# Performance work log

Hardware: AMD Instinct MI355X
Metric: run time of the kernel (lower is better)

Reference implementation:

```python
import jax, jax.numpy as jnp
import numpy as np

NUM_HEAD = 8

def setup_inputs() -> dict:
    key = jax.random.key(0)
    ks = jax.random.split(key, 5)
    S, F, H = 4096, 1024, 1024
    scale = 0.02
    return {
        "x": jax.random.normal(ks[0], (1, S, F), dtype=jnp.float32),
        "Wq": jax.random.normal(ks[1], (F, H), dtype=jnp.float32) * scale,
        "Wk": jax.random.normal(ks[2], (F, H), dtype=jnp.float32) * scale,
        "Wv": jax.random.normal(ks[3], (F, H), dtype=jnp.float32) * scale,
        "Wo": jax.random.normal(ks[4], (H, F), dtype=jnp.float32) * scale,
    }

def reference(x, Wq, Wk, Wv, Wo):
    # x: [1, S, F]; weights applied as x @ W (torch Linear bias=False equivalent).
    # Dropout layers are treated as identity (eval mode) for determinism.
    B, S, F = x.shape
    H = Wq.shape[1]
    d_k = H // NUM_HEAD
    q = (x @ Wq).reshape(S, NUM_HEAD, d_k).transpose(1, 0, 2)  # [h, S, d_k]
    k = (x @ Wk).reshape(S, NUM_HEAD, d_k).transpose(1, 0, 2)
    v = (x @ Wv).reshape(S, NUM_HEAD, d_k).transpose(1, 0, 2)
    # Full attention matrix materialized, matching the original bmm-softmax-bmm.
    attn = jnp.einsum("hsd,htd->hst", q, k) / jnp.sqrt(jnp.float32(d_k))  # [h, S, S]
    attn = jax.nn.softmax(attn, axis=-1)
    y = jnp.einsum("hst,htd->hsd", attn, v)  # [h, S, d_k]
    y = y.transpose(1, 0, 2).reshape(1, S, H)  # [1, S, H]
    y = y @ Wo  # output projection [1, S, F]
    return (y, attn)
```

## Files before the change

kernel.cpp:

```cpp
#include <hip/hip_runtime.h>
#include <math.h>


typedef unsigned short u16;
typedef __attribute__((ext_vector_type(8))) short bf16x8;
typedef __attribute__((ext_vector_type(4))) float f32x4;

#define SEQ 4096
#define FDIM 1024
#define NHEAD 8
#define DK 128

__device__ __forceinline__ u16 f2bf(float f) {
  unsigned u = __float_as_uint(f);
  u += 0x7fffu + ((u >> 16) & 1u);
  return (u16)(u >> 16);
}
__device__ __forceinline__ float bf2f(u16 h) {
  return __uint_as_float(((unsigned)h) << 16);
}

__device__ __forceinline__ void g2l16(const void* g, void* l) {
  __builtin_amdgcn_global_load_lds(
      (const __attribute__((address_space(1))) void*)g,
      (__attribute__((address_space(3))) void*)l, 16, 0, 0);
}


__global__ void split_f32_bf16(const float4* __restrict__ in, u16* __restrict__ ohi,
                               u16* __restrict__ olo, int n4) {
  int i = blockIdx.x * 256 + threadIdx.x;
  if (i >= n4) return;
  float4 v = in[i];
  u16 h0 = f2bf(v.x), h1 = f2bf(v.y), h2 = f2bf(v.z), h3 = f2bf(v.w);
  u16 l0 = f2bf(v.x - bf2f(h0)), l1 = f2bf(v.y - bf2f(h1));
  u16 l2 = f2bf(v.z - bf2f(h2)), l3 = f2bf(v.w - bf2f(h3));
  *(ushort4*)(ohi + 4 * (size_t)i) = make_ushort4(h0, h1, h2, h3);
  *(ushort4*)(olo + 4 * (size_t)i) = make_ushort4(l0, l1, l2, l3);
}

__global__ void transpose_split_w(const float* __restrict__ in, u16* __restrict__ ohi,
                                  u16* __restrict__ olo, int dim, int do_split) {
  __shared__ float t[32][33];
  int tx = threadIdx.x, ty = threadIdx.y;
  int x = blockIdx.x * 32 + tx;
  int y0 = blockIdx.y * 32;
  for (int j = ty; j < 32; j += 8) t[j][tx] = in[(long)(y0 + j) * dim + x];
  __syncthreads();
  int x2 = y0 + tx;
  int y2 = blockIdx.x * 32;
  for (int j = ty; j < 32; j += 8) {
    float v = t[tx][j];
    u16 hi = f2bf(v);
    ohi[(long)(y2 + j) * dim + x2] = hi;
    if (do_split) olo[(long)(y2 + j) * dim + x2] = f2bf(v - bf2f(hi));
  }
}

__global__ void transpose_bf16(const u16* __restrict__ in, u16* __restrict__ out,
                               int rows, int cols) {
  __shared__ u16 t[32][33];
  int tx = threadIdx.x, ty = threadIdx.y;
  int x = blockIdx.x * 32 + tx;
  int y0 = blockIdx.y * 32;
  for (int j = ty; j < 32; j += 8) t[j][tx] = in[(long)(y0 + j) * cols + x];
  __syncthreads();
  int x2 = y0 + tx;
  int y2 = blockIdx.x * 32;
  for (int j = ty; j < 32; j += 8) out[(long)(y2 + j) * rows + x2] = t[tx][j];
}

__global__ void reciprocal_k(const float* __restrict__ in, float* __restrict__ out, int n) {
  int i = blockIdx.x * 256 + threadIdx.x;
  if (i < n) out[i] = 1.0f / in[i];
}

template <int BK, bool SPLIT, int EPI>
__global__ __launch_bounds__(256, 2) void gemm_bt(
    const u16* Ahi_, const u16* Alo_,
    const u16* Bhi_, const u16* Blo_,
    void* C0, void* C1,
    int Kdim, int lda, int ldb, int ldc,
    long aStrH, long bStrH, long cStrH) {
  constexpr int LDSN = 128 * BK;
  __shared__ u16 sAhi[LDSN];
  __shared__ u16 sBhi[LDSN];
  __shared__ u16 sAlo[SPLIT ? LDSN : 2];
  __shared__ u16 sBlo[SPLIT ? LDSN : 2];

  const int tid = threadIdx.x;
  const int lane = tid & 63;
  const int wave = tid >> 6;
  const int wr = wave >> 1, wc = wave & 1;
  const int quad = lane >> 4, l16 = lane & 15;
  const int h = blockIdx.z;
  const long bm = (long)blockIdx.y * 128;
  const long bn = (long)blockIdx.x * 128;

  const u16* Ahi = Ahi_ + (long)h * aStrH;
  const u16* Alo = SPLIT ? (Alo_ + (long)h * aStrH) : nullptr;
  const u16* Bhi = Bhi_ + (long)h * bStrH;
  const u16* Blo = SPLIT ? (Blo_ + (long)h * bStrH) : nullptr;

  f32x4 acc[4][4];
#pragma unroll
  for (int i = 0; i < 4; i++)
#pragma unroll
    for (int j = 0; j < 4; j++) acc[i][j] = (f32x4)0.0f;

  for (int k0 = 0; k0 < Kdim; k0 += BK) {
    constexpr int GR = (128 * BK) / (256 * 8);
#pragma unroll
    for (int r = 0; r < GR; ++r) {
      int e = (r * 256 + tid) * 8;
      int row = e / BK, col = e % BK;
      long ga = (bm + row) * (long)lda + k0 + col;
      long gb = (bn + row) * (long)ldb + k0 + col;
      g2l16(Ahi + ga, (char*)sAhi + (size_t)e * 2);
      g2l16(Bhi + gb, (char*)sBhi + (size_t)e * 2);
      if constexpr (SPLIT) {
        g2l16(Alo + ga, (char*)sAlo + (size_t)e * 2);
        g2l16(Blo + gb, (char*)sBlo + (size_t)e * 2);
      }
    }
    __syncthreads();

#pragma unroll
    for (int ks = 0; ks < BK; ks += 32) {
      bf16x8 aH[4], bH[4];
      bf16x8 aL[SPLIT ? 4 : 1], bL[SPLIT ? 4 : 1];
#pragma unroll
      for (int mi = 0; mi < 4; mi++) {
        int off = (wr * 64 + mi * 16 + l16) * BK + ks + quad * 8;
        aH[mi] = *(const bf16x8*)&sAhi[off];
        if constexpr (SPLIT) aL[mi] = *(const bf16x8*)&sAlo[off];
      }
#pragma unroll
      for (int ni = 0; ni < 4; ni++) {
        int off = (wc * 64 + ni * 16 + l16) * BK + ks + quad * 8;
        bH[ni] = *(const bf16x8*)&sBhi[off];
        if constexpr (SPLIT) bL[ni] = *(const bf16x8*)&sBlo[off];
      }
#pragma unroll
      for (int mi = 0; mi < 4; mi++)
#pragma unroll
        for (int ni = 0; ni < 4; ni++) {
          acc[mi][ni] = __builtin_amdgcn_mfma_f32_16x16x32_bf16(aH[mi], bH[ni], acc[mi][ni], 0, 0, 0);
          if constexpr (SPLIT) {
            acc[mi][ni] = __builtin_amdgcn_mfma_f32_16x16x32_bf16(aH[mi], bL[ni], acc[mi][ni], 0, 0, 0);
            acc[mi][ni] = __builtin_amdgcn_mfma_f32_16x16x32_bf16(aL[mi], bH[ni], acc[mi][ni], 0, 0, 0);
          }
        }
    }
    __syncthreads();
  }

  const long rowB = bm + wr * 64;
  const long colB = bn + wc * 64;
  if constexpr (EPI == 2) {
    u16* Chi = (u16*)C0 + (long)h * cStrH;
    u16* Clo = (u16*)C1 + (long)h * cStrH;
#pragma unroll
    for (int mi = 0; mi < 4; mi++)
#pragma unroll
      for (int ni = 0; ni < 4; ni++) {
        long col = colB + ni * 16 + l16;
#pragma unroll
        for (int r = 0; r < 4; r++) {
          long idx = (rowB + mi * 16 + quad * 4 + r) * (long)ldc + col;
          float v = acc[mi][ni][r];
          u16 hi = f2bf(v);
          Chi[idx] = hi;
          Clo[idx] = f2bf(v - bf2f(hi));
        }
      }
  } else if constexpr (EPI == 1) {
    u16* C = (u16*)C0 + (long)h * cStrH;
#pragma unroll
    for (int mi = 0; mi < 4; mi++)
#pragma unroll
      for (int ni = 0; ni < 4; ni++) {
        long col = colB + ni * 16 + l16;
#pragma unroll
        for (int r = 0; r < 4; r++)
          C[(rowB + mi * 16 + quad * 4 + r) * (long)ldc + col] = f2bf(acc[mi][ni][r]);
      }
  } else {
    float* C = (float*)C0 + (long)h * cStrH;
#pragma unroll
    for (int mi = 0; mi < 4; mi++)
#pragma unroll
      for (int ni = 0; ni < 4; ni++) {
        long col = colB + ni * 16 + l16;
#pragma unroll
        for (int r = 0; r < 4; r++)
          C[(rowB + mi * 16 + quad * 4 + r) * (long)ldc + col] = acc[mi][ni][r];
      }
  }
}

template <bool BF16S>
__global__ __launch_bounds__(256, 2) void qk_exp(
    const u16* __restrict__ Qhi, const u16* __restrict__ Qlo,
    const u16* __restrict__ Khi, const u16* __restrict__ Klo,
    void* __restrict__ outE, float* __restrict__ rowSum, float scale) {
  __shared__ u16 smem[32768];
  u16* sQh = smem;
  u16* sQl = smem + 8192;
  u16* sKh = smem + 16384;
  u16* sKl = smem + 24576;

  const int tid = threadIdx.x;
  const int lane = tid & 63, wave = tid >> 6;
  const int wr = wave >> 1, wc = wave & 1;
  const int quad = lane >> 4, l16 = lane & 15;
  const int h = blockIdx.z;
  const int bm = blockIdx.y * 128, bn = blockIdx.x * 128;
  const int colOff = h * DK;

  f32x4 acc[4][4];
#pragma unroll
  for (int i = 0; i < 4; i++)
#pragma unroll
    for (int j = 0; j < 4; j++) acc[i][j] = (f32x4)0.0f;

  for (int k0 = 0; k0 < DK; k0 += 64) {
#pragma unroll
    for (int r = 0; r < 4; ++r) {
      int e = (r * 256 + tid) * 8;
      int row = e >> 6, col = e & 63;
      long gq = (long)(bm + row) * FDIM + colOff + k0 + col;
      long gk = (long)(bn + row) * FDIM + colOff + k0 + col;
      g2l16(Qhi + gq, (char*)sQh + (size_t)e * 2);
      g2l16(Qlo + gq, (char*)sQl + (size_t)e * 2);
      g2l16(Khi + gk, (char*)sKh + (size_t)e * 2);
      g2l16(Klo + gk, (char*)sKl + (size_t)e * 2);
    }
    __syncthreads();
#pragma unroll
    for (int ks = 0; ks < 64; ks += 32) {
      bf16x8 aH[4], aL[4], bH[4], bL[4];
#pragma unroll
      for (int i = 0; i < 4; i++) {
        int offA = (wr * 64 + i * 16 + l16) * 64 + ks + quad * 8;
        int offB = (wc * 64 + i * 16 + l16) * 64 + ks + quad * 8;
        aH[i] = *(const bf16x8*)&sQh[offA];
        aL[i] = *(const bf16x8*)&sQl[offA];
        bH[i] = *(const bf16x8*)&sKh[offB];
        bL[i] = *(const bf16x8*)&sKl[offB];
      }
#pragma unroll
      for (int mi = 0; mi < 4; mi++)
#pragma unroll
        for (int ni = 0; ni < 4; ni++) {
          acc[mi][ni] = __builtin_amdgcn_mfma_f32_16x16x32_bf16(aH[mi], bH[ni], acc[mi][ni], 0, 0, 0);
          acc[mi][ni] = __builtin_amdgcn_mfma_f32_16x16x32_bf16(aH[mi], bL[ni], acc[mi][ni], 0, 0, 0);
          acc[mi][ni] = __builtin_amdgcn_mfma_f32_16x16x32_bf16(aL[mi], bH[ni], acc[mi][ni], 0, 0, 0);
        }
    }
    __syncthreads();
  }

#pragma unroll
  for (int mi = 0; mi < 4; mi++) {
    f32x4 rs = (f32x4)0.0f;
#pragma unroll
    for (int ni = 0; ni < 4; ni++)
#pragma unroll
      for (int r = 0; r < 4; r++) {
        float e = __expf(acc[mi][ni][r] * scale);
        acc[mi][ni][r] = e;
        rs[r] += e;
      }
#pragma unroll
    for (int m = 1; m < 16; m <<= 1) {
      rs[0] += __shfl_xor(rs[0], m);
      rs[1] += __shfl_xor(rs[1], m);
      rs[2] += __shfl_xor(rs[2], m);
      rs[3] += __shfl_xor(rs[3], m);
    }
    if (l16 == 0) {
      int rbase = h * SEQ + bm + wr * 64 + mi * 16 + quad * 4;
#pragma unroll
      for (int r = 0; r < 4; r++) atomicAdd(&rowSum[rbase + r], rs[r]);
    }
  }

  u16* P = smem;
#pragma unroll
  for (int mi = 0; mi < 4; mi++)
#pragma unroll
    for (int ni = 0; ni < 4; ni++)
#pragma unroll
      for (int r = 0; r < 4; r++)
        P[(wr * 64 + mi * 16 + quad * 4 + r) * 128 + wc * 64 + ni * 16 + l16] =
            f2bf(acc[mi][ni][r]);
  __syncthreads();

  if constexpr (BF16S) {
    u16* out = (u16*)outE + ((long)h << 24);
#pragma unroll
    for (int j = 0; j < 8; ++j) {
      int e = (j * 256 + tid) * 8;
      int row = e >> 7, col = e & 127;
      long g = (long)(bm + row) * SEQ + bn + col;
      *(uint4*)(out + g) = *(const uint4*)(P + e);
    }
  } else {
    float* out = (float*)outE + ((long)h << 24);
#pragma unroll
    for (int j = 0; j < 16; ++j) {
      int e = (j * 256 + tid) * 4;
      int row = e >> 7, col = e & 127;
      long g = (long)(bm + row) * SEQ + bn + col;
      ushort4 u = *(const ushort4*)(P + e);
      *(float4*)(out + g) = make_float4(bf2f(u.x), bf2f(u.y), bf2f(u.z), bf2f(u.w));
    }
  }
}

template <bool BF16S>
__global__ __launch_bounds__(256, 2) void pv_norm(
    const void* __restrict__ expS, const float* __restrict__ invRow,
    float* __restrict__ attnOut, const u16* __restrict__ Vt,
    u16* __restrict__ Yb) {
  __shared__ u16 sP[2][64 * 64];
  __shared__ u16 sV[2][128 * 64];
  const int tid = threadIdx.x;
  const int lane = tid & 63, wave = tid >> 6;
  const int wr = wave >> 1, wc = wave & 1;
  const int quad = lane >> 4, l16 = lane & 15;
  const int h = blockIdx.z;
  const int bm = blockIdx.y * 64;

  const int e0 = tid * 8, e1 = (256 + tid) * 8;
  const int row0 = e0 >> 6, col0 = e0 & 63;
  const int row1 = e1 >> 6, col1 = e1 & 63;
  const long arow0 = (long)h * SEQ + bm + row0;
  const long arow1 = (long)h * SEQ + bm + row1;
  const float inv0 = invRow[arow0];
  const float inv1 = invRow[arow1];

  f32x4 acc[2][4];
#pragma unroll
  for (int i = 0; i < 2; i++)
#pragma unroll
    for (int j = 0; j < 4; j++) acc[i][j] = (f32x4)0.0f;

  bf16x8 pbA0, pbA1, pbB0, pbB1;
  f32x4 pfA0, pfA1, pfA2, pfA3, pfB0, pfB1, pfB2, pfB3;

#define LOADP(S, k0)                                                           \
  do {                                                                         \
    if constexpr (BF16S) {                                                     \
      const u16* _s = (const u16*)expS;                                        \
      pb##S##0 = __builtin_nontemporal_load(                                   \
          (const bf16x8*)(_s + arow0 * SEQ + (k0) + col0));                    \
      pb##S##1 = __builtin_nontemporal_load(                                   \
          (const bf16x8*)(_s + arow1 * SEQ + (k0) + col1));                    \
    } else {                                                                   \
      const float* _s = (const float*)expS;                                    \
      pf##S##0 = __builtin_nontemporal_load(                                   \
          (const f32x4*)(_s + arow0 * SEQ + (k0) + col0));                     \
      pf##S##1 = __builtin_nontemporal_load(                                   \
          (const f32x4*)(_s + arow0 * SEQ + (k0) + col0 + 4));                 \
      pf##S##2 = __builtin_nontemporal_load(                                   \
          (const f32x4*)(_s + arow1 * SEQ + (k0) + col1));                     \
      pf##S##3 = __builtin_nontemporal_load(                                   \
          (const f32x4*)(_s + arow1 * SEQ + (k0) + col1 + 4));                 \
    }                                                                          \
  } while (0)

#define PROC(S, k0, buf)                                                       \
  do {                                                                         \
    float p0[8], p1[8];                                                        \
    if constexpr (BF16S) {                                                     \
      p0[0] = bf2f((u16)pb##S##0[0]) * inv0;                                   \
      p0[1] = bf2f((u16)pb##S##0[1]) * inv0;                                   \
      p0[2] = bf2f((u16)pb##S##0[2]) * inv0;                                   \
      p0[3] = bf2f((u16)pb##S##0[3]) * inv0;                                   \
      p0[4] = bf2f((u16)pb##S##0[4]) * inv0;                                   \
      p0[5] = bf2f((u16)pb##S##0[5]) * inv0;                                   \
      p0[6] = bf2f((u16)pb##S##0[6]) * inv0;                                   \
      p0[7] = bf2f((u16)pb##S##0[7]) * inv0;                                   \
      p1[0] = bf2f((u16)pb##S##1[0]) * inv1;                                   \
      p1[1] = bf2f((u16)pb##S##1[1]) * inv1;                                   \
      p1[2] = bf2f((u16)pb##S##1[2]) * inv1;                                   \
      p1[3] = bf2f((u16)pb##S##1[3]) * inv1;                                   \
      p1[4] = bf2f((u16)pb##S##1[4]) * inv1;                                   \
      p1[5] = bf2f((u16)pb##S##1[5]) * inv1;                                   \
      p1[6] = bf2f((u16)pb##S##1[6]) * inv1;                                   \
      p1[7] = bf2f((u16)pb##S##1[7]) * inv1;                                   \
    } else {                                                                   \
      p0[0] = pf##S##0[0] * inv0; p0[1] = pf##S##0[1] * inv0;                  \
      p0[2] = pf##S##0[2] * inv0; p0[3] = pf##S##0[3] * inv0;                  \
      p0[4] = pf##S##1[0] * inv0; p0[5] = pf##S##1[1] * inv0;                  \
      p0[6] = pf##S##1[2] * inv0; p0[7] = pf##S##1[3] * inv0;                  \
      p1[0] = pf##S##2[0] * inv1; p1[1] = pf##S##2[1] * inv1;                  \
      p1[2] = pf##S##2[2] * inv1; p1[3] = pf##S##2[3] * inv1;                  \
      p1[4] = pf##S##3[0] * inv1; p1[5] = pf##S##3[1] * inv1;                  \
      p1[6] = pf##S##3[2] * inv1; p1[7] = pf##S##3[3] * inv1;                  \
    }                                                                          \
    long _g0 = arow0 * SEQ + (k0) + col0;                                      \
    long _g1 = arow1 * SEQ + (k0) + col1;                                      \
    f32x4 _w0 = {p0[0], p0[1], p0[2], p0[3]};                                  \
    f32x4 _w1 = {p0[4], p0[5], p0[6], p0[7]};                                  \
    f32x4 _w2 = {p1[0], p1[1], p1[2], p1[3]};                                  \
    f32x4 _w3 = {p1[4], p1[5], p1[6], p1[7]};                                  \
    __builtin_nontemporal_store(_w0, (f32x4*)(attnOut + _g0));                 \
    __builtin_nontemporal_store(_w1, (f32x4*)(attnOut + _g0 + 4));             \
    __builtin_nontemporal_store(_w2, (f32x4*)(attnOut + _g1));                 \
    __builtin_nontemporal_store(_w3, (f32x4*)(attnOut + _g1 + 4));             \
    *(ushort4*)(sP[buf] + e0) =                                                \
        make_ushort4(f2bf(p0[0]), f2bf(p0[1]), f2bf(p0[2]), f2bf(p0[3]));      \
    *(ushort4*)(sP[buf] + e0 + 4) =                                            \
        make_ushort4(f2bf(p0[4]), f2bf(p0[5]), f2bf(p0[6]), f2bf(p0[7]));      \
    *(ushort4*)(sP[buf] + e1) =                                                \
        make_ushort4(f2bf(p1[0]), f2bf(p1[1]), f2bf(p1[2]), f2bf(p1[3]));      \
    *(ushort4*)(sP[buf] + e1 + 4) =                                            \
        make_ushort4(f2bf(p1[4]), f2bf(p1[5]), f2bf(p1[6]), f2bf(p1[7]));      \
  } while (0)

  auto STAGEV = [&](int k0, int buf) {
#pragma unroll
    for (int r = 0; r < 4; ++r) {
      int e = (r * 256 + tid) * 8;
      int row = e >> 6, col = e & 63;
      g2l16(Vt + (long)(h * DK + row) * SEQ + k0 + col,
            (char*)sV[buf] + (size_t)e * 2);
    }
  };

  auto DO_MFMA = [&](int buf) {
#pragma unroll
    for (int ks = 0; ks < 64; ks += 32) {
      bf16x8 a[2], b[4];
#pragma unroll
      for (int i = 0; i < 2; i++)
        a[i] = *(const bf16x8*)&sP[buf][(wr * 32 + i * 16 + l16) * 64 + ks + quad * 8];
#pragma unroll
      for (int i = 0; i < 4; i++)
        b[i] = *(const bf16x8*)&sV[buf][(wc * 64 + i * 16 + l16) * 64 + ks + quad * 8];
#pragma unroll
      for (int mi = 0; mi < 2; mi++)
#pragma unroll
        for (int ni = 0; ni < 4; ni++)
          acc[mi][ni] = __builtin_amdgcn_mfma_f32_16x16x32_bf16(a[mi], b[ni], acc[mi][ni], 0, 0, 0);
    }
  };

  LOADP(A, 0);
  STAGEV(0, 0);
  LOADP(B, 64);
  PROC(A, 0, 0);
  __syncthreads();

  for (int it = 0; it < 62; it += 2) {
    LOADP(A, (it + 2) * 64);
    STAGEV((it + 1) * 64, 1);
    DO_MFMA(0);
    PROC(B, (it + 1) * 64, 1);
    __syncthreads();
    LOADP(B, (it + 3) * 64);
    STAGEV((it + 2) * 64, 0);
    DO_MFMA(1);
    PROC(A, (it + 2) * 64, 0);
    __syncthreads();
  }
  STAGEV(63 * 64, 1);
  DO_MFMA(0);
  PROC(B, 63 * 64, 1);
  __syncthreads();
  DO_MFMA(1);

#undef LOADP
#undef PROC

#pragma unroll
  for (int mi = 0; mi < 2; mi++)
#pragma unroll
    for (int ni = 0; ni < 4; ni++)
#pragma unroll
      for (int r = 0; r < 4; r++) {
        long row = bm + wr * 32 + mi * 16 + quad * 4 + r;
        int col = h * DK + wc * 64 + ni * 16 + l16;
        Yb[row * (long)FDIM + col] = f2bf(acc[mi][ni][r]);
      }
}


extern "C" void kernel_launch(void* const* d_in, const int* in_sizes, int n_in,
                              void* d_out, int out_size, void* d_ws, size_t ws_size,
                              hipStream_t stream) {
  const float* x = (const float*)d_in[0];
  const float* Wq = (const float*)d_in[1];
  const float* Wk = (const float*)d_in[2];
  const float* Wv = (const float*)d_in[3];
  const float* Wo = (const float*)d_in[4];

  float* outY = (float*)d_out;
  float* attn = outY + (size_t)SEQ * FDIM;

  const size_t NX = (size_t)SEQ * FDIM;
  const size_t NW = (size_t)FDIM * FDIM;

  u16* p = (u16*)d_ws;
  u16* xhi = p; p += NX;
  u16* xlo = p; p += NX;
  u16* wqt_h = p; p += NW;
  u16* wqt_l = p; p += NW;
  u16* wkt_h = p; p += NW;
  u16* wkt_l = p; p += NW;
  u16* wvt = p; p += NW;
  u16* wot = p; p += NW;
  u16* Qhi = p; p += NX;
  u16* Qlo = p; p += NX;
  u16* Khi = p; p += NX;
  u16* Klo = p; p += NX;
  u16* Vb = p; p += NX;
  u16* Vt = p; p += NX;
  u16* Yb = p; p += NX;
  float* rowSum = (float*)p;
  float* invRow = rowSum + (size_t)NHEAD * SEQ;
  u16* expS = (u16*)(invRow + (size_t)NHEAD * SEQ);
  size_t need = (size_t)((char*)(expS + (size_t)NHEAD * SEQ * SEQ) - (char*)d_ws);
  bool bf16s = ws_size >= need;

  hipMemsetAsync(rowSum, 0, (size_t)NHEAD * SEQ * sizeof(float), stream);

  split_f32_bf16<<<dim3((NX / 4 + 255) / 256), 256, 0, stream>>>(
      (const float4*)x, xhi, xlo, NX / 4);

  dim3 tb(32, 8);
  transpose_split_w<<<dim3(32, 32), tb, 0, stream>>>(Wq, wqt_h, wqt_l, FDIM, 1);
  transpose_split_w<<<dim3(32, 32), tb, 0, stream>>>(Wk, wkt_h, wkt_l, FDIM, 1);
  transpose_split_w<<<dim3(32, 32), tb, 0, stream>>>(Wv, wvt, nullptr, FDIM, 0);
  transpose_split_w<<<dim3(32, 32), tb, 0, stream>>>(Wo, wot, nullptr, FDIM, 0);

  gemm_bt<32, true, 2><<<dim3(8, 32, 2), 256, 0, stream>>>(
      xhi, xlo, wqt_h, wqt_l, Qhi, Qlo,
      1024, 1024, 1024, 1024, 0, (long)2 * NW, (long)2 * NX);

  gemm_bt<64, false, 1><<<dim3(8, 32, 1), 256, 0, stream>>>(
      xhi, nullptr, wvt, nullptr, Vb, nullptr,
      1024, 1024, 1024, 1024, 0, 0, 0);
  transpose_bf16<<<dim3(32, 128), tb, 0, stream>>>(Vb, Vt, SEQ, FDIM);

  const float scale = 0.08838834764831845f;
  if (bf16s) {
    qk_exp<true><<<dim3(32, 32, NHEAD), 256, 0, stream>>>(
        Qhi, Qlo, Khi, Klo, expS, rowSum, scale);
  } else {
    qk_exp<false><<<dim3(32, 32, NHEAD), 256, 0, stream>>>(
        Qhi, Qlo, Khi, Klo, attn, rowSum, scale);
  }

  reciprocal_k<<<(NHEAD * SEQ + 255) / 256, 256, 0, stream>>>(rowSum, invRow, NHEAD * SEQ);

  if (bf16s) {
    pv_norm<true><<<dim3(1, 64, NHEAD), 256, 0, stream>>>(expS, invRow, attn, Vt, Yb);
  } else {
    pv_norm<false><<<dim3(1, 64, NHEAD), 256, 0, stream>>>(attn, invRow, attn, Vt, Yb);
  }

  gemm_bt<64, false, 0><<<dim3(8, 32, 1), 256, 0, stream>>>(
      Yb, nullptr, wot, nullptr, outY, nullptr,
      1024, 1024, 1024, 1024, 0, 0, 0);
}
```

Before: 1.170 ms.

## Split PV product into split-K GEMM, reduction, and separate attention normalization

On the bf16 path, the fused PV-and-normalize kernel is replaced by three kernels. First, a split-K GEMM over the unnormalized exp scores with larger 128-row tiles writes fp32 partials into the attn buffer as scratch. Second, a reduction applies the per-row reciprocal and converts to bf16. Third, a standalone streaming kernel writes the normalized fp32 attention matrix. This aims to raise parallelism and MFMA tile efficiency beyond the 512-block grid, at the cost of rereading expS, extra partial traffic, and more launches. The fp32 fallback pv_norm loses its double-buffered pipeline.

Measured after the change: 1.270 ms. +8.5%, slower.

```diff
diff --git a/kernel.cpp b/kernel.cpp
--- a/kernel.cpp
+++ b/kernel.cpp
@@ -4,12 +4,14 @@
 
 typedef unsigned short u16;
 typedef __attribute__((ext_vector_type(8))) short bf16x8;
+typedef __attribute__((ext_vector_type(8))) unsigned short u16x8;
 typedef __attribute__((ext_vector_type(4))) float f32x4;
 
 #define SEQ 4096
 #define FDIM 1024
 #define NHEAD 8
 #define DK 128
+#define KSPLIT 4
 
 __device__ __forceinline__ u16 f2bf(float f) {
   unsigned u = __float_as_uint(f);
@@ -319,13 +321,113 @@
   }
 }
 
+__global__ __launch_bounds__(256, 4) void pv_gemm(
+    const u16* __restrict__ expS, const u16* __restrict__ Vt,
+    float* __restrict__ ypart) {
+  __shared__ u16 sA[128 * 64];
+  __shared__ u16 sB[128 * 64];
+  const int tid = threadIdx.x;
+  const int lane = tid & 63, wave = tid >> 6;
+  const int wr = wave >> 1, wc = wave & 1;
+  const int quad = lane >> 4, l16 = lane & 15;
+  const int h = blockIdx.z;
+  const long bm = (long)blockIdx.y * 128;
+  const int kBase = blockIdx.x * (SEQ / KSPLIT);
+
+  const u16* A = expS + ((long)h << 24);
+  const u16* B = Vt + (long)h * DK * SEQ;
+
+  f32x4 acc[4][4];
+#pragma unroll
+  for (int i = 0; i < 4; i++)
+#pragma unroll
+    for (int j = 0; j < 4; j++) acc[i][j] = (f32x4)0.0f;
+
+  for (int k0 = kBase; k0 < kBase + SEQ / KSPLIT; k0 += 64) {
+#pragma unroll
+    for (int r = 0; r < 4; ++r) {
+      int e = (r * 256 + tid) * 8;
+      int row = e >> 6, col = e & 63;
+      g2l16(A + (bm + row) * (long)SEQ + k0 + col, (char*)sA + (size_t)e * 2);
+      g2l16(B + (long)row * SEQ + k0 + col, (char*)sB + (size_t)e * 2);
+    }
+    __syncthreads();
+#pragma unroll
+    for (int ks = 0; ks < 64; ks += 32) {
+      bf16x8 a[4], b[4];
+#pragma unroll
+      for (int mi = 0; mi < 4; mi++)
+        a[mi] = *(const bf16x8*)&sA[(wr * 64 + mi * 16 + l16) * 64 + ks + quad * 8];
+#pragma unroll
+      for (int ni = 0; ni < 4; ni++)
+        b[ni] = *(const bf16x8*)&sB[(wc * 64 + ni * 16 + l16) * 64 + ks + quad * 8];
+#pragma unroll
+      for (int mi = 0; mi < 4; mi++)
+#pragma unroll
+        for (int ni = 0; ni < 4; ni++)
+          acc[mi][ni] = __builtin_amdgcn_mfma_f32_16x16x32_bf16(a[mi], b[ni], acc[mi][ni], 0, 0, 0);
+    }
+    __syncthreads();
+  }
+
+  float* out = ypart + (long)blockIdx.x * ((long)SEQ * FDIM);
+#pragma unroll
+  for (int mi = 0; mi < 4; mi++)
+#pragma unroll
+    for (int ni = 0; ni < 4; ni++) {
+      int col = h * DK + wc * 64 + ni * 16 + l16;
+#pragma unroll
+      for (int r = 0; r < 4; r++) {
+        long row = bm + wr * 64 + mi * 16 + quad * 4 + r;
+        out[row * (long)FDIM + col] = acc[mi][ni][r];
+      }
+    }
+}
+
+__global__ void y_reduce_scale(const float* __restrict__ ypart,
+                               const float* __restrict__ invRow,
+                               u16* __restrict__ Yb) {
+  long i = ((long)blockIdx.x * 256 + threadIdx.x) * 4;
+  int s = (int)(i >> 10);
+  int f = (int)(i & 1023);
+  float inv = invRow[(f >> 7) * SEQ + s];
+  const long NP = (long)SEQ * FDIM;
+  f32x4 v = *(const f32x4*)(ypart + i);
+#pragma unroll
+  for (int ks = 1; ks < KSPLIT; ks++) v = v + *(const f32x4*)(ypart + ks * NP + i);
+  *(ushort4*)(Yb + i) =
+      make_ushort4(f2bf(v[0] * inv), f2bf(v[1] * inv), f2bf(v[2] * inv), f2bf(v[3] * inv));
+}
+
+__global__ void attn_norm(const u16* __restrict__ expS,
+                          const float* __restrict__ invRow,
+                          float* __restrict__ attn) {
+  const long TOT = ((long)NHEAD << 24) >> 4;
+  long c = (long)blockIdx.x * 256 + threadIdx.x;
+  const long stride = (long)gridDim.x * 256;
+  for (; c < TOT; c += stride) {
+    long flat = c << 4;
+    float inv = invRow[flat >> 12];
+    u16x8 v0 = __builtin_nontemporal_load((const u16x8*)(expS + flat));
+    u16x8 v1 = __builtin_nontemporal_load((const u16x8*)(expS + flat + 8));
+    f32x4 w0 = {bf2f(v0[0]) * inv, bf2f(v0[1]) * inv, bf2f(v0[2]) * inv, bf2f(v0[3]) * inv};
+    f32x4 w1 = {bf2f(v0[4]) * inv, bf2f(v0[5]) * inv, bf2f(v0[6]) * inv, bf2f(v0[7]) * inv};
+    f32x4 w2 = {bf2f(v1[0]) * inv, bf2f(v1[1]) * inv, bf2f(v1[2]) * inv, bf2f(v1[3]) * inv};
+    f32x4 w3 = {bf2f(v1[4]) * inv, bf2f(v1[5]) * inv, bf2f(v1[6]) * inv, bf2f(v1[7]) * inv};
+    __builtin_nontemporal_store(w0, (f32x4*)(attn + flat));
+    __builtin_nontemporal_store(w1, (f32x4*)(attn + flat + 4));
+    __builtin_nontemporal_store(w2, (f32x4*)(attn + flat + 8));
+    __builtin_nontemporal_store(w3, (f32x4*)(attn + flat + 12));
+  }
+}
+
 template <bool BF16S>
 __global__ __launch_bounds__(256, 2) void pv_norm(
     const void* __restrict__ expS, const float* __restrict__ invRow,
     float* __restrict__ attnOut, const u16* __restrict__ Vt,
     u16* __restrict__ Yb) {
-  __shared__ u16 sP[2][64 * 64];
-  __shared__ u16 sV[2][128 * 64];
+  __shared__ u16 sP[64 * 64];
+  __shared__ u16 sV[128 * 64];
   const int tid = threadIdx.x;
   const int lane = tid & 63, wave = tid >> 6;
   const int wr = wave >> 1, wc = wave & 1;
@@ -333,148 +435,63 @@
   const int h = blockIdx.z;
   const int bm = blockIdx.y * 64;
 
-  const int e0 = tid * 8, e1 = (256 + tid) * 8;
-  const int row0 = e0 >> 6, col0 = e0 & 63;
-  const int row1 = e1 >> 6, col1 = e1 & 63;
-  const long arow0 = (long)h * SEQ + bm + row0;
-  const long arow1 = (long)h * SEQ + bm + row1;
-  const float inv0 = invRow[arow0];
-  const float inv1 = invRow[arow1];
-
   f32x4 acc[2][4];
 #pragma unroll
   for (int i = 0; i < 2; i++)
 #pragma unroll
     for (int j = 0; j < 4; j++) acc[i][j] = (f32x4)0.0f;
 
-  bf16x8 pbA0, pbA1, pbB0, pbB1;
-  f32x4 pfA0, pfA1, pfA2, pfA3, pfB0, pfB1, pfB2, pfB3;
-
-#define LOADP(S, k0)                                                           \
-  do {                                                                         \
-    if constexpr (BF16S) {                                                     \
-      const u16* _s = (const u16*)expS;                                        \
-      pb##S##0 = __builtin_nontemporal_load(                                   \
-          (const bf16x8*)(_s + arow0 * SEQ + (k0) + col0));                    \
-      pb##S##1 = __builtin_nontemporal_load(                                   \
-          (const bf16x8*)(_s + arow1 * SEQ + (k0) + col1));                    \
-    } else {                                                                   \
-      const float* _s = (const float*)expS;                                    \
-      pf##S##0 = __builtin_nontemporal_load(                                   \
-          (const f32x4*)(_s + arow0 * SEQ + (k0) + col0));                     \
-      pf##S##1 = __builtin_nontemporal_load(                                   \
-          (const f32x4*)(_s + arow0 * SEQ + (k0) + col0 + 4));                 \
-      pf##S##2 = __builtin_nontemporal_load(                                   \
-          (const f32x4*)(_s + arow1 * SEQ + (k0) + col1));                     \
-      pf##S##3 = __builtin_nontemporal_load(                                   \
-          (const f32x4*)(_s + arow1 * SEQ + (k0) + col1 + 4));                 \
-    }                                                                          \
-  } while (0)
-
-#define PROC(S, k0, buf)                                                       \
-  do {                                                                         \
-    float p0[8], p1[8];                                                        \
-    if constexpr (BF16S) {                                                     \
-      p0[0] = bf2f((u16)pb##S##0[0]) * inv0;                                   \
-      p0[1] = bf2f((u16)pb##S##0[1]) * inv0;                                   \
-      p0[2] = bf2f((u16)pb##S##0[2]) * inv0;                                   \
-      p0[3] = bf2f((u16)pb##S##0[3]) * inv0;                                   \
-      p0[4] = bf2f((u16)pb##S##0[4]) * inv0;                                   \
-      p0[5] = bf2f((u16)pb##S##0[5]) * inv0;                                   \
-      p0[6] = bf2f((u16)pb##S##0[6]) * inv0;                                   \
-      p0[7] = bf2f((u16)pb##S##0[7]) * inv0;                                   \
-      p1[0] = bf2f((u16)pb##S##1[0]) * inv1;                                   \
-      p1[1] = bf2f((u16)pb##S##1[1]) * inv1;                                   \
-      p1[2] = bf2f((u16)pb##S##1[2]) * inv1;                                   \
-      p1[3] = bf2f((u16)pb##S##1[3]) * inv1;                                   \
-      p1[4] = bf2f((u16)pb##S##1[4]) * inv1;                                   \
-      p1[5] = bf2f((u16)pb##S##1[5]) * inv1;                                   \
-      p1[6] = bf2f((u16)pb##S##1[6]) * inv1;                                   \
-      p1[7] = bf2f((u16)pb##S##1[7]) * inv1;                                   \
-    } else {                                                                   \
-      p0[0] = pf##S##0[0] * inv0; p0[1] = pf##S##0[1] * inv0;                  \
-      p0[2] = pf##S##0[2] * inv0; p0[3] = pf##S##0[3] * inv0;                  \
-      p0[4] = pf##S##1[0] * inv0; p0[5] = pf##S##1[1] * inv0;                  \
-      p0[6] = pf##S##1[2] * inv0; p0[7] = pf##S##1[3] * inv0;                  \
-      p1[0] = pf##S##2[0] * inv1; p1[1] = pf##S##2[1] * inv1;                  \
-      p1[2] = pf##S##2[2] * inv1; p1[3] = pf##S##2[3] * inv1;                  \
-      p1[4] = pf##S##3[0] * inv1; p1[5] = pf##S##3[1] * inv1;                  \
-      p1[6] = pf##S##3[2] * inv1; p1[7] = pf##S##3[3] * inv1;                  \
-    }                                                                          \
-    long _g0 = arow0 * SEQ + (k0) + col0;                                      \
-    long _g1 = arow1 * SEQ + (k0) + col1;                                      \
-    f32x4 _w0 = {p0[0], p0[1], p0[2], p0[3]};                                  \
-    f32x4 _w1 = {p0[4], p0[5], p0[6], p0[7]};                                  \
-    f32x4 _w2 = {p1[0], p1[1], p1[2], p1[3]};                                  \
-    f32x4 _w3 = {p1[4], p1[5], p1[6], p1[7]};                                  \
-    __builtin_nontemporal_store(_w0, (f32x4*)(attnOut + _g0));                 \
-    __builtin_nontemporal_store(_w1, (f32x4*)(attnOut + _g0 + 4));             \
-    __builtin_nontemporal_store(_w2, (f32x4*)(attnOut + _g1));                 \
-    __builtin_nontemporal_store(_w3, (f32x4*)(attnOut + _g1 + 4));             \
-    *(ushort4*)(sP[buf] + e0) =                                                \
-        make_ushort4(f2bf(p0[0]), f2bf(p0[1]), f2bf(p0[2]), f2bf(p0[3]));      \
-    *(ushort4*)(sP[buf] + e0 + 4) =                                            \
-        make_ushort4(f2bf(p0[4]), f2bf(p0[5]), f2bf(p0[6]), f2bf(p0[7]));      \
-    *(ushort4*)(sP[buf] + e1) =                                                \
-        make_ushort4(f2bf(p1[0]), f2bf(p1[1]), f2bf(p1[2]), f2bf(p1[3]));      \
-    *(ushort4*)(sP[buf] + e1 + 4) =                                            \
-        make_ushort4(f2bf(p1[4]), f2bf(p1[5]), f2bf(p1[6]), f2bf(p1[7]));      \
-  } while (0)
-
-  auto STAGEV = [&](int k0, int buf) {
+  for (int k0 = 0; k0 < SEQ; k0 += 64) {
+#pragma unroll
+    for (int c = 0; c < 2; ++c) {
+      int e = (c * 256 + tid) * 8;
+      int row = e >> 6, col = e & 63;
+      long arow = (long)h * SEQ + bm + row;
+      long g = arow * SEQ + k0 + col;
+      float inv = invRow[arow];
+      float p[8];
+      if constexpr (BF16S) {
+        ushort4 u0 = *(const ushort4*)((const u16*)expS + g);
+        ushort4 u1 = *(const ushort4*)((const u16*)expS + g + 4);
+        p[0] = bf2f(u0.x) * inv; p[1] = bf2f(u0.y) * inv;
+        p[2] = bf2f(u0.z) * inv; p[3] = bf2f(u0.w) * inv;
+        p[4] = bf2f(u1.x) * inv; p[5] = bf2f(u1.y) * inv;
+        p[6] = bf2f(u1.z) * inv; p[7] = bf2f(u1.w) * inv;
+      } else {
+        float4 f0 = *(const float4*)((const float*)expS + g);
+        float4 f1 = *(const float4*)((const float*)expS + g + 4);
+        p[0] = f0.x * inv; p[1] = f0.y * inv; p[2] = f0.z * inv; p[3] = f0.w * inv;
+        p[4] = f1.x * inv; p[5] = f1.y * inv; p[6] = f1.z * inv; p[7] = f1.w * inv;
+      }
+      *(float4*)(attnOut + g) = make_float4(p[0], p[1], p[2], p[3]);
+      *(float4*)(attnOut + g + 4) = make_float4(p[4], p[5], p[6], p[7]);
+      *(ushort4*)(sP + e) = make_ushort4(f2bf(p[0]), f2bf(p[1]), f2bf(p[2]), f2bf(p[3]));
+      *(ushort4*)(sP + e + 4) = make_ushort4(f2bf(p[4]), f2bf(p[5]), f2bf(p[6]), f2bf(p[7]));
+    }
 #pragma unroll
     for (int r = 0; r < 4; ++r) {
       int e = (r * 256 + tid) * 8;
       int row = e >> 6, col = e & 63;
-      g2l16(Vt + (long)(h * DK + row) * SEQ + k0 + col,
-            (char*)sV[buf] + (size_t)e * 2);
-    }
-  };
-
-  auto DO_MFMA = [&](int buf) {
+      g2l16(Vt + (long)(h * DK + row) * SEQ + k0 + col, (char*)sV + (size_t)e * 2);
+    }
+    __syncthreads();
 #pragma unroll
     for (int ks = 0; ks < 64; ks += 32) {
       bf16x8 a[2], b[4];
 #pragma unroll
       for (int i = 0; i < 2; i++)
-        a[i] = *(const bf16x8*)&sP[buf][(wr * 32 + i * 16 + l16) * 64 + ks + quad * 8];
+        a[i] = *(const bf16x8*)&sP[(wr * 32 + i * 16 + l16) * 64 + ks + quad * 8];
 #pragma unroll
       for (int i = 0; i < 4; i++)
-        b[i] = *(const bf16x8*)&sV[buf][(wc * 64 + i * 16 + l16) * 64 + ks + quad * 8];
+        b[i] = *(const bf16x8*)&sV[(wc * 64 + i * 16 + l16) * 64 + ks + quad * 8];
 #pragma unroll
       for (int mi = 0; mi < 2; mi++)
 #pragma unroll
         for (int ni = 0; ni < 4; ni++)
           acc[mi][ni] = __builtin_amdgcn_mfma_f32_16x16x32_bf16(a[mi], b[ni], acc[mi][ni], 0, 0, 0);
     }
-  };
-
-  LOADP(A, 0);
-  STAGEV(0, 0);
-  LOADP(B, 64);
-  PROC(A, 0, 0);
-  __syncthreads();
-
-  for (int it = 0; it < 62; it += 2) {
-    LOADP(A, (it + 2) * 64);
-    STAGEV((it + 1) * 64, 1);
-    DO_MFMA(0);
-    PROC(B, (it + 1) * 64, 1);
-    __syncthreads();
-    LOADP(B, (it + 3) * 64);
-    STAGEV((it + 2) * 64, 0);
-    DO_MFMA(1);
-    PROC(A, (it + 2) * 64, 0);
-    __syncthreads();
-  }
-  STAGEV(63 * 64, 1);
-  DO_MFMA(0);
-  PROC(B, 63 * 64, 1);
-  __syncthreads();
-  DO_MFMA(1);
-
-#undef LOADP
-#undef PROC
+    __syncthreads();
+  }
 
 #pragma unroll
   for (int mi = 0; mi < 2; mi++)
@@ -550,16 +567,16 @@
   if (bf16s) {
     qk_exp<true><<<dim3(32, 32, NHEAD), 256, 0, stream>>>(
         Qhi, Qlo, Khi, Klo, expS, rowSum, scale);
+    reciprocal_k<<<(NHEAD * SEQ + 255) / 256, 256, 0, stream>>>(rowSum, invRow, NHEAD * SEQ);
+
+    float* ypart = attn;
+    pv_gemm<<<dim3(KSPLIT, 32, NHEAD), 256, 0, stream>>>(expS, Vt, ypart);
+    y_reduce_scale<<<dim3(NX / 4 / 256), 256, 0, stream>>>(ypart, invRow, Yb);
+    attn_norm<<<dim3(2048), 256, 0, stream>>>(expS, invRow, attn);
   } else {
     qk_exp<false><<<dim3(32, 32, NHEAD), 256, 0, stream>>>(
         Qhi, Qlo, Khi, Klo, attn, rowSum, scale);
-  }
-
-  reciprocal_k<<<(NHEAD * SEQ + 255) / 256, 256, 0, stream>>>(rowSum, invRow, NHEAD * SEQ);
-
-  if (bf16s) {
-    pv_norm<true><<<dim3(1, 64, NHEAD), 256, 0, stream>>>(expS, invRow, attn, Vt, Yb);
-  } else {
+    reciprocal_k<<<(NHEAD * SEQ + 255) / 256, 256, 0, stream>>>(rowSum, invRow, NHEAD * SEQ);
     pv_norm<false><<<dim3(1, 64, NHEAD), 256, 0, stream>>>(attn, invRow, attn, Vt, Yb);
   }
 
```
